# Performance work log

Measured on AMD Instinct MI355X. Metric: run time of the kernel, lower is better.

Reference implementation:

```python
import jax, jax.numpy as jnp
import numpy as np

N_NODES = 50000
N_EDGES = 1600000
NFEAT, NHID, NCLASS = 512, 128, 40


def spmm(rows, cols, vals, dense, n_rows):
    # COO sparse @ dense: gather source rows, scale, scatter-add into dest rows.
    msgs = dense[cols] * vals[:, None]            # [E, F]
    return jax.ops.segment_sum(msgs, rows, num_segments=n_rows)  # [N, F]


def setup_inputs() -> dict:
    key = jax.random.key(0)
    ks = jax.random.split(key, 10)
    s1 = 1.0 / np.sqrt(NFEAT)
    s2 = 1.0 / np.sqrt(NHID)
    return {
        "x": jax.random.normal(ks[0], (N_NODES, NFEAT), jnp.float32),
        "adj_rows": jax.random.randint(ks[1], (N_EDGES,), 0, N_NODES, jnp.int32),
        "adj_cols": jax.random.randint(ks[2], (N_EDGES,), 0, N_NODES, jnp.int32),
        "adj_vals": jax.random.uniform(ks[3], (N_EDGES,), jnp.float32) * 0.05,
        "W1": jax.random.normal(ks[4], (NFEAT, NHID), jnp.float32) * s1,
        "b1": jnp.zeros((NHID,), jnp.float32),
        "W2": jax.random.normal(ks[5], (NHID, NHID), jnp.float32) * s2,
        "b2": jnp.zeros((NHID,), jnp.float32),
        "Wout": jax.random.normal(ks[6], (NHID, NCLASS), jnp.float32) * s2,
        "bout": jnp.zeros((NCLASS,), jnp.float32),
    }


def reference(x, adj_rows, adj_cols, adj_vals, W1, b1, W2, b2, Wout, bout):
    n = x.shape[0]
    # GraphConvolution 1: support = x @ W1; out = spmm(adj, support) + b1; relu
    h = jax.nn.relu(spmm(adj_rows, adj_cols, adj_vals, x @ W1, n) + b1)
    # dropout: inference mode (training=False) -> identity
    # GraphConvolution 2 (same adjacency), relu
    h = jax.nn.relu(spmm(adj_rows, adj_cols, adj_vals, h @ W2, n) + b2)
    # output linear + log_softmax over classes
    logits = h @ Wout + bout
    return jax.nn.log_softmax(logits, axis=1)
```

## Files before the change

kernel.cpp:

```cpp
#include <hip/hip_runtime.h>

#define NFEAT 512
#define NHID 128
#define NCLASS 40
#define CAP 80

__global__ __launch_bounds__(512)
void gemm_k(const float* __restrict__ A, const float* __restrict__ B,
            float* __restrict__ C, int M, int K) {
    __shared__ float As[64][32];
    __shared__ float Bs[32][128];
    const int tid = threadIdx.x;
    const int m0  = blockIdx.x * 64;
    const int tr  = tid >> 5;
    const int tc  = tid & 31;
    const int la_r = tid >> 3;
    const int la_c = (tid & 7) << 2;
    const int lb_r = tid >> 5;
    const int lb_c = (tid & 31) << 2;

    float acc[4][4] = {};

    for (int k0 = 0; k0 < K; k0 += 32) {
        {
            int m  = m0 + la_r;
            int ms = m < M ? m : (M - 1);
            *(float4*)&As[la_r][la_c] =
                *(const float4*)(A + (size_t)ms * K + k0 + la_c);
        }
        #pragma unroll
        for (int h = 0; h < 2; ++h) {
            int kr = lb_r + h * 16;
            *(float4*)&Bs[kr][lb_c] = *(const float4*)(B + (size_t)(k0 + kr) * 128 + lb_c);
        }
        __syncthreads();

        #pragma unroll
        for (int kk = 0; kk < 8; ++kk) {
            float4 a4[4];
            #pragma unroll
            for (int i = 0; i < 4; ++i)
                a4[i] = *(const float4*)&As[tr + i * 16][kk * 4];
            #pragma unroll
            for (int kq = 0; kq < 4; ++kq) {
                const int k = kk * 4 + kq;
                float b[4];
                #pragma unroll
                for (int j = 0; j < 4; ++j) b[j] = Bs[k][tc + j * 32];
                #pragma unroll
                for (int i = 0; i < 4; ++i) {
                    const float av = (kq == 0) ? a4[i].x : (kq == 1) ? a4[i].y
                                   : (kq == 2) ? a4[i].z : a4[i].w;
                    #pragma unroll
                    for (int j = 0; j < 4; ++j)
                        acc[i][j] = fmaf(av, b[j], acc[i][j]);
                }
            }
        }
        __syncthreads();
    }

    #pragma unroll
    for (int i = 0; i < 4; ++i) {
        int m = m0 + tr + i * 16;
        if (m < M) {
            #pragma unroll
            for (int j = 0; j < 4; ++j)
                C[(size_t)m * 128 + tc + j * 32] = acc[i][j];
        }
    }
}

__global__ __launch_bounds__(256)
void build_k(const int* __restrict__ rows, const int* __restrict__ cols,
             const float* __restrict__ vals, int* __restrict__ deg,
             int2* __restrict__ ccv, int E) {
    int e = blockIdx.x * 256 + threadIdx.x;
    if (e >= E) return;
    int r = rows[e];
    int k = atomicAdd(&deg[r], 1);
    if (k < CAP)
        ccv[(size_t)r * CAP + k] = make_int2(cols[e], __float_as_int(vals[e]));
}

__global__ __launch_bounds__(256)
void hist_k(const int* __restrict__ rows, int* __restrict__ deg, int E) {
    int e = blockIdx.x * 256 + threadIdx.x;
    if (e < E) atomicAdd(&deg[rows[e]], 1);
}

__global__ __launch_bounds__(1024)
void scan_k(const int* __restrict__ deg, int* __restrict__ rowptr,
            int* __restrict__ pos, int N) {
    __shared__ int partial[1024];
    const int t = threadIdx.x;
    const int chunk = (N + 1023) >> 10;
    const int lo = t * chunk;
    const int hi = min(N, lo + chunk);
    int s = 0;
    for (int i = lo; i < hi; ++i) s += deg[i];
    partial[t] = s;
    __syncthreads();
    for (int off = 1; off < 1024; off <<= 1) {
        int v = 0;
        if (t >= off) v = partial[t - off];
        __syncthreads();
        if (t >= off) partial[t] += v;
        __syncthreads();
    }
    int base = (t == 0) ? 0 : partial[t - 1];
    for (int i = lo; i < hi; ++i) {
        rowptr[i] = base;
        pos[i]    = base;
        base += deg[i];
    }
    if (t == 0) rowptr[N] = partial[1023];
}

__global__ __launch_bounds__(256)
void scatter_k(const int* __restrict__ rows, const int* __restrict__ cols,
               const float* __restrict__ vals, int* __restrict__ pos,
               int2* __restrict__ ccv, int E) {
    int e = blockIdx.x * 256 + threadIdx.x;
    if (e >= E) return;
    int p = atomicAdd(&pos[rows[e]], 1);
    ccv[p] = make_int2(cols[e], __float_as_int(vals[e]));
}

template<bool PAD>
__global__ __launch_bounds__(256)
void spmm_mid_k(const int* __restrict__ rp, const int2* __restrict__ ccv,
                const float* __restrict__ src, const float* __restrict__ bias,
                float* __restrict__ dst, int N) {
    int row = (blockIdx.x * 256 + threadIdx.x) >> 6;
    const int lane = threadIdx.x & 63;
    if (row >= N) return;
    row = __builtin_amdgcn_readfirstlane(row);
    int start, cnt;
    if (PAD) { start = row * CAP; cnt = min(rp[row], CAP); }
    else     { start = rp[row];   cnt = rp[row + 1] - start; }
    const int2* __restrict__ p = ccv + start;
    const int fo = lane << 1;
    float2 acc = {0.f, 0.f};
    int j = 0;
    for (; j + 7 < cnt; j += 8) {
        int2 cv[8];
        #pragma unroll
        for (int u = 0; u < 8; ++u) cv[u] = p[j + u];
        float2 s[8];
        #pragma unroll
        for (int u = 0; u < 8; ++u)
            s[u] = *(const float2*)(src + (cv[u].x << 7) + fo);
        #pragma unroll
        for (int u = 0; u < 8; ++u) {
            float v = __int_as_float(cv[u].y);
            acc.x = fmaf(v, s[u].x, acc.x); acc.y = fmaf(v, s[u].y, acc.y);
        }
    }
    for (; j < cnt; ++j) {
        int2 cv = p[j];
        float v = __int_as_float(cv.y);
        float2 s = *(const float2*)(src + (cv.x << 7) + fo);
        acc.x = fmaf(v, s.x, acc.x); acc.y = fmaf(v, s.y, acc.y);
    }
    float2 bv = *(const float2*)(bias + fo);
    acc.x = fmaxf(acc.x + bv.x, 0.f);
    acc.y = fmaxf(acc.y + bv.y, 0.f);
    *(float2*)(dst + (size_t)row * NHID + fo) = acc;
}

template<bool PAD>
__global__ __launch_bounds__(256)
void spmm_out_k(const int* __restrict__ rp, const int2* __restrict__ ccv,
                const float* __restrict__ src, const float* __restrict__ b2,
                const float* __restrict__ Wout, const float* __restrict__ bout,
                float* __restrict__ out, int N) {
    __shared__ float Ws[NHID * NCLASS];
    __shared__ float hs[4][NHID];
    const int tid = threadIdx.x;
    for (int i = tid; i < NHID * NCLASS; i += 256) Ws[i] = Wout[i];
    __syncthreads();

    int row = (blockIdx.x * 256 + tid) >> 6;
    const int wave = tid >> 6, lane = tid & 63;
    if (row >= N) return;
    row = __builtin_amdgcn_readfirstlane(row);
    int start, cnt;
    if (PAD) { start = row * CAP; cnt = min(rp[row], CAP); }
    else     { start = rp[row];   cnt = rp[row + 1] - start; }
    const int2* __restrict__ p = ccv + start;
    const int fo = lane << 1;
    float2 acc = {0.f, 0.f};
    int j = 0;
    for (; j + 7 < cnt; j += 8) {
        int2 cv[8];
        #pragma unroll
        for (int u = 0; u < 8; ++u) cv[u] = p[j + u];
        float2 s[8];
        #pragma unroll
        for (int u = 0; u < 8; ++u)
            s[u] = *(const float2*)(src + (cv[u].x << 7) + fo);
        #pragma unroll
        for (int u = 0; u < 8; ++u) {
            float v = __int_as_float(cv[u].y);
            acc.x = fmaf(v, s[u].x, acc.x); acc.y = fmaf(v, s[u].y, acc.y);
        }
    }
    for (; j < cnt; ++j) {
        int2 cv = p[j];
        float v = __int_as_float(cv.y);
        float2 s = *(const float2*)(src + (cv.x << 7) + fo);
        acc.x = fmaf(v, s.x, acc.x); acc.y = fmaf(v, s.y, acc.y);
    }
    float2 bv = *(const float2*)(b2 + fo);
    hs[wave][fo]     = fmaxf(acc.x + bv.x, 0.f);
    hs[wave][fo + 1] = fmaxf(acc.y + bv.y, 0.f);

    float logit = -INFINITY;
    if (lane < NCLASS) {
        logit = bout[lane];
        #pragma unroll 4
        for (int k = 0; k < NHID; ++k)
            logit = fmaf(hs[wave][k], Ws[k * NCLASS + lane], logit);
    }
    float m = logit;
    #pragma unroll
    for (int o = 32; o > 0; o >>= 1) m = fmaxf(m, __shfl_xor(m, o));
    float e = (lane < NCLASS) ? expf(logit - m) : 0.f;
    float s = e;
    #pragma unroll
    for (int o = 32; o > 0; o >>= 1) s += __shfl_xor(s, o);
    const float lse = logf(s);
    if (lane < NCLASS)
        out[(size_t)row * NCLASS + lane] = logit - m - lse;
}

__global__ __launch_bounds__(256)
void spmm_coo_k(const int* __restrict__ rows, const int* __restrict__ cols,
                const float* __restrict__ vals, const float* __restrict__ src,
                float* __restrict__ dst, int E) {
    const long long t = (long long)blockIdx.x * 256 + threadIdx.x;
    const int e = (int)(t >> 5);
    if (e >= E) return;
    const int c = ((int)t & 31) << 2;
    const float4 s4 = *(const float4*)(src + ((size_t)cols[e] << 7) + c);
    const float v = vals[e];
    float* d = dst + ((size_t)rows[e] << 7) + c;
    unsafeAtomicAdd(d + 0, s4.x * v);
    unsafeAtomicAdd(d + 1, s4.y * v);
    unsafeAtomicAdd(d + 2, s4.z * v);
    unsafeAtomicAdd(d + 3, s4.w * v);
}

__global__ __launch_bounds__(256)
void relu_bias_k(float* __restrict__ h, const float* __restrict__ b, int total) {
    int i = blockIdx.x * 256 + threadIdx.x;
    if (i < total) h[i] = fmaxf(h[i] + b[i & (NHID - 1)], 0.f);
}

__global__ __launch_bounds__(256)
void out_k(const float* __restrict__ h2, const float* __restrict__ b2,
           const float* __restrict__ Wout, const float* __restrict__ bout,
           float* __restrict__ out, int M) {
    __shared__ float Ws[NHID * NCLASS];
    __shared__ float hs[4][NHID];
    const int tid = threadIdx.x;
    for (int i = tid; i < NHID * NCLASS; i += 256) Ws[i] = Wout[i];
    const int wave = tid >> 6, lane = tid & 63;
    const int row = blockIdx.x * 4 + wave;
    if (row < M) {
        #pragma unroll
        for (int c = lane; c < NHID; c += 64)
            hs[wave][c] = fmaxf(h2[(size_t)row * NHID + c] + b2[c], 0.f);
    }
    __syncthreads();
    if (row >= M) return;
    float acc = -INFINITY;
    if (lane < NCLASS) {
        acc = bout[lane];
        #pragma unroll 4
        for (int k = 0; k < NHID; ++k)
            acc = fmaf(hs[wave][k], Ws[k * NCLASS + lane], acc);
    }
    float m = acc;
    #pragma unroll
    for (int o = 32; o > 0; o >>= 1) m = fmaxf(m, __shfl_xor(m, o));
    float e = (lane < NCLASS) ? expf(acc - m) : 0.f;
    float s = e;
    #pragma unroll
    for (int o = 32; o > 0; o >>= 1) s += __shfl_xor(s, o);
    const float lse = logf(s);
    if (lane < NCLASS)
        out[(size_t)row * NCLASS + lane] = acc - m - lse;
}

extern "C" void kernel_launch(void* const* d_in, const int* in_sizes, int n_in,
                              void* d_out, int out_size, void* d_ws, size_t ws_size,
                              hipStream_t stream) {
    const float* x     = (const float*)d_in[0];
    const int*   arows = (const int*)  d_in[1];
    const int*   acols = (const int*)  d_in[2];
    const float* avals = (const float*)d_in[3];
    const float* W1    = (const float*)d_in[4];
    const float* b1    = (const float*)d_in[5];
    const float* W2    = (const float*)d_in[6];
    const float* b2    = (const float*)d_in[7];
    const float* Wout  = (const float*)d_in[8];
    const float* bout  = (const float*)d_in[9];
    float* out = (float*)d_out;

    const int M = in_sizes[0] / NFEAT;
    const int E = in_sizes[1];

    const size_t hbytes = (size_t)M * NHID * sizeof(float);
    char* wp = (char*)d_ws;
    float* bufA = (float*)wp;  wp += hbytes;
    float* bufB = (float*)wp;  wp += hbytes;
    int*   deg  = (int*)wp;    wp += (size_t)M * sizeof(int);
    char*  tail = wp;

    const size_t need_pad = (size_t)(tail - (char*)d_ws) + (size_t)M * CAP * sizeof(int2);
    const size_t need_csr = (size_t)(tail - (char*)d_ws) + ((size_t)M + 1 + M) * sizeof(int)
                          + (size_t)E * sizeof(int2);

    gemm_k<<<(M + 63) / 64, 512, 0, stream>>>(x, W1, bufA, M, NFEAT);

    if (need_pad <= ws_size) {
        int2* ccv = (int2*)tail;
        hipMemsetAsync(deg, 0, (size_t)M * sizeof(int), stream);
        build_k<<<(E + 255) / 256, 256, 0, stream>>>(arows, acols, avals, deg, ccv, E);
        spmm_mid_k<true><<<(M * 64 + 255) / 256, 256, 0, stream>>>(deg, ccv, bufA, b1, bufB, M);
        gemm_k<<<(M + 63) / 64, 512, 0, stream>>>(bufB, W2, bufA, M, NHID);
        spmm_out_k<true><<<(M * 64 + 255) / 256, 256, 0, stream>>>(deg, ccv, bufA, b2, Wout, bout, out, M);
    } else if (need_csr <= ws_size) {
        int* rowptr = (int*)tail;
        int* pos    = rowptr + (M + 1);
        int2* ccv   = (int2*)(pos + M);
        hipMemsetAsync(deg, 0, (size_t)M * sizeof(int), stream);
        hist_k   <<<(E + 255) / 256, 256, 0, stream>>>(arows, deg, E);
        scan_k   <<<1, 1024, 0, stream>>>(deg, rowptr, pos, M);
        scatter_k<<<(E + 255) / 256, 256, 0, stream>>>(arows, acols, avals, pos, ccv, E);
        spmm_mid_k<false><<<(M * 64 + 255) / 256, 256, 0, stream>>>(rowptr, ccv, bufA, b1, bufB, M);
        gemm_k<<<(M + 63) / 64, 512, 0, stream>>>(bufB, W2, bufA, M, NHID);
        spmm_out_k<false><<<(M * 64 + 255) / 256, 256, 0, stream>>>(rowptr, ccv, bufA, b2, Wout, bout, out, M);
    } else {
        hipMemsetAsync(bufB, 0, hbytes, stream);
        spmm_coo_k<<<(E * 32 + 255) / 256, 256, 0, stream>>>(arows, acols, avals, bufA, bufB, E);
        relu_bias_k<<<((M * NHID) + 255) / 256, 256, 0, stream>>>(bufB, b1, M * NHID);
        gemm_k<<<(M + 63) / 64, 512, 0, stream>>>(bufB, W2, bufA, M, NHID);
        hipMemsetAsync(bufB, 0, hbytes, stream);
        spmm_coo_k<<<(E * 32 + 255) / 256, 256, 0, stream>>>(arows, acols, avals, bufA, bufB, E);
        out_k<<<(M + 3) / 4, 256, 0, stream>>>(bufB, b2, Wout, bout, out, M);
    }
}
```

Baseline: 609.4 us.

## Store intermediate node features in fp16 and retile GEMM to 8x4 per thread

The intermediate feature buffers (support and hidden activations) become half precision, which halves the bytes moved by the random row gathers in both SpMM kernels and by the GEMM stores. Accumulation still happens in fp32. The GEMM drops to 256 threads, each computing an 8x4 output tile with float4 reads from shared memory, and can now load fp16 A input. The COO atomic fallback path is removed, so the CSR path becomes the unconditional fallback. This trades some accuracy for less memory traffic, and with a small workspace the fallback could now overrun it.

```diff
diff --git a/kernel.cpp b/kernel.cpp
--- a/kernel.cpp
+++ b/kernel.cpp
@@ -1,59 +1,71 @@
 #include <hip/hip_runtime.h>
+#include <hip/hip_fp16.h>
+#include <type_traits>
 
 #define NFEAT 512
 #define NHID 128
 #define NCLASS 40
 #define CAP 80
 
-__global__ __launch_bounds__(512)
-void gemm_k(const float* __restrict__ A, const float* __restrict__ B,
-            float* __restrict__ C, int M, int K) {
+template<typename TA>
+__global__ __launch_bounds__(256)
+void gemm_k(const TA* __restrict__ A, const float* __restrict__ B,
+            __half* __restrict__ C, int M, int K) {
     __shared__ float As[64][32];
     __shared__ float Bs[32][128];
     const int tid = threadIdx.x;
     const int m0  = blockIdx.x * 64;
-    const int tr  = tid >> 5;
-    const int tc  = tid & 31;
+    const int ty  = tid >> 5;
+    const int tx  = tid & 31;
     const int la_r = tid >> 3;
     const int la_c = (tid & 7) << 2;
     const int lb_r = tid >> 5;
     const int lb_c = (tid & 31) << 2;
 
-    float acc[4][4] = {};
+    float acc[8][4] = {};
 
     for (int k0 = 0; k0 < K; k0 += 32) {
-        {
-            int m  = m0 + la_r;
+        #pragma unroll
+        for (int h = 0; h < 2; ++h) {
+            int m  = m0 + la_r + h * 32;
             int ms = m < M ? m : (M - 1);
-            *(float4*)&As[la_r][la_c] =
-                *(const float4*)(A + (size_t)ms * K + k0 + la_c);
-        }
-        #pragma unroll
-        for (int h = 0; h < 2; ++h) {
-            int kr = lb_r + h * 16;
+            if constexpr (std::is_same<TA, float>::value) {
+                *(float4*)&As[la_r + h * 32][la_c] =
+                    *(const float4*)(A + (size_t)ms * K + k0 + la_c);
+            } else {
+                const __half2* ap = (const __half2*)(A + (size_t)ms * K + k0 + la_c);
+                float2 f0 = __half22float2(ap[0]);
+                float2 f1 = __half22float2(ap[1]);
+                *(float4*)&As[la_r + h * 32][la_c] = make_float4(f0.x, f0.y, f1.x, f1.y);
+            }
+        }
+        #pragma unroll
+        for (int h = 0; h < 4; ++h) {
+            int kr = lb_r + h * 8;
             *(float4*)&Bs[kr][lb_c] = *(const float4*)(B + (size_t)(k0 + kr) * 128 + lb_c);
         }
         __syncthreads();
 
         #pragma unroll
         for (int kk = 0; kk < 8; ++kk) {
-            float4 a4[4];
+            float4 a4[8];
             #pragma unroll
-            for (int i = 0; i < 4; ++i)
-                a4[i] = *(const float4*)&As[tr + i * 16][kk * 4];
+            for (int i = 0; i < 8; ++i)
+                a4[i] = *(const float4*)&As[ty * 8 + i][kk * 4];
+            float4 bb[4];
             #pragma unroll
-            for (int kq = 0; kq < 4; ++kq) {
-                const int k = kk * 4 + kq;
-                float b[4];
+            for (int q = 0; q < 4; ++q)
+                bb[q] = *(const float4*)&Bs[kk * 4 + q][tx * 4];
+            #pragma unroll
+            for (int q = 0; q < 4; ++q) {
                 #pragma unroll
-                for (int j = 0; j < 4; ++j) b[j] = Bs[k][tc + j * 32];
-                #pragma unroll
-                for (int i = 0; i < 4; ++i) {
-                    const float av = (kq == 0) ? a4[i].x : (kq == 1) ? a4[i].y
-                                   : (kq == 2) ? a4[i].z : a4[i].w;
-                    #pragma unroll
-                    for (int j = 0; j < 4; ++j)
-                        acc[i][j] = fmaf(av, b[j], acc[i][j]);
+                for (int i = 0; i < 8; ++i) {
+                    const float av = (q == 0) ? a4[i].x : (q == 1) ? a4[i].y
+                                   : (q == 2) ? a4[i].z : a4[i].w;
+                    acc[i][0] = fmaf(av, bb[q].x, acc[i][0]);
+                    acc[i][1] = fmaf(av, bb[q].y, acc[i][1]);
+                    acc[i][2] = fmaf(av, bb[q].z, acc[i][2]);
+                    acc[i][3] = fmaf(av, bb[q].w, acc[i][3]);
                 }
             }
         }
@@ -61,12 +73,15 @@
     }
 
     #pragma unroll
-    for (int i = 0; i < 4; ++i) {
-        int m = m0 + tr + i * 16;
+    for (int i = 0; i < 8; ++i) {
+        int m = m0 + ty * 8 + i;
         if (m < M) {
-            #pragma unroll
-            for (int j = 0; j < 4; ++j)
-                C[(size_t)m * 128 + tc + j * 32] = acc[i][j];
+            __half2 lo = __floats2half2_rn(acc[i][0], acc[i][1]);
+            __half2 hi = __floats2half2_rn(acc[i][2], acc[i][3]);
+            int2 pk;
+            *(__half2*)&pk.x = lo;
+            *(__half2*)&pk.y = hi;
+            *(int2*)(C + (size_t)m * 128 + tx * 4) = pk;
         }
     }
 }
@@ -130,8 +145,8 @@
 template<bool PAD>
 __global__ __launch_bounds__(256)
 void spmm_mid_k(const int* __restrict__ rp, const int2* __restrict__ ccv,
-                const float* __restrict__ src, const float* __restrict__ bias,
-                float* __restrict__ dst, int N) {
+                const __half* __restrict__ src, const float* __restrict__ bias,
+                __half* __restrict__ dst, int N) {
     int row = (blockIdx.x * 256 + threadIdx.x) >> 6;
     const int lane = threadIdx.x & 63;
     if (row >= N) return;
@@ -150,7 +165,7 @@
         float2 s[8];
         #pragma unroll
         for (int u = 0; u < 8; ++u)
-            s[u] = *(const float2*)(src + (cv[u].x << 7) + fo);
+            s[u] = __half22float2(*(const __half2*)(src + (cv[u].x << 7) + fo));
         #pragma unroll
         for (int u = 0; u < 8; ++u) {
             float v = __int_as_float(cv[u].y);
@@ -160,19 +175,19 @@
     for (; j < cnt; ++j) {
         int2 cv = p[j];
         float v = __int_as_float(cv.y);
-        float2 s = *(const float2*)(src + (cv.x << 7) + fo);
+        float2 s = __half22float2(*(const __half2*)(src + (cv.x << 7) + fo));
         acc.x = fmaf(v, s.x, acc.x); acc.y = fmaf(v, s.y, acc.y);
     }
     float2 bv = *(const float2*)(bias + fo);
     acc.x = fmaxf(acc.x + bv.x, 0.f);
     acc.y = fmaxf(acc.y + bv.y, 0.f);
-    *(float2*)(dst + (size_t)row * NHID + fo) = acc;
+    *(__half2*)(dst + (size_t)row * NHID + fo) = __floats2half2_rn(acc.x, acc.y);
 }
 
 template<bool PAD>
 __global__ __launch_bounds__(256)
 void spmm_out_k(const int* __restrict__ rp, const int2* __restrict__ ccv,
-                const float* __restrict__ src, const float* __restrict__ b2,
+                const __half* __restrict__ src, const float* __restrict__ b2,
                 const float* __restrict__ Wout, const float* __restrict__ bout,
                 float* __restrict__ out, int N) {
     __shared__ float Ws[NHID * NCLASS];
@@ -199,7 +214,7 @@
         float2 s[8];
         #pragma unroll
         for (int u = 0; u < 8; ++u)
-            s[u] = *(const float2*)(src + (cv[u].x << 7) + fo);
+            s[u] = __half22float2(*(const __half2*)(src + (cv[u].x << 7) + fo));
         #pragma unroll
         for (int u = 0; u < 8; ++u) {
             float v = __int_as_float(cv[u].y);
@@ -209,7 +224,7 @@
     for (; j < cnt; ++j) {
         int2 cv = p[j];
         float v = __int_as_float(cv.y);
-        float2 s = *(const float2*)(src + (cv.x << 7) + fo);
+        float2 s = __half22float2(*(const __half2*)(src + (cv.x << 7) + fo));
         acc.x = fmaf(v, s.x, acc.x); acc.y = fmaf(v, s.y, acc.y);
     }
     float2 bv = *(const float2*)(b2 + fo);
@@ -233,65 +248,6 @@
     const float lse = logf(s);
     if (lane < NCLASS)
         out[(size_t)row * NCLASS + lane] = logit - m - lse;
-}
-
-__global__ __launch_bounds__(256)
-void spmm_coo_k(const int* __restrict__ rows, const int* __restrict__ cols,
-                const float* __restrict__ vals, const float* __restrict__ src,
-                float* __restrict__ dst, int E) {
-    const long long t = (long long)blockIdx.x * 256 + threadIdx.x;
-    const int e = (int)(t >> 5);
-    if (e >= E) return;
-    const int c = ((int)t & 31) << 2;
-    const float4 s4 = *(const float4*)(src + ((size_t)cols[e] << 7) + c);
-    const float v = vals[e];
-    float* d = dst + ((size_t)rows[e] << 7) + c;
-    unsafeAtomicAdd(d + 0, s4.x * v);
-    unsafeAtomicAdd(d + 1, s4.y * v);
-    unsafeAtomicAdd(d + 2, s4.z * v);
-    unsafeAtomicAdd(d + 3, s4.w * v);
-}
-
-__global__ __launch_bounds__(256)
-void relu_bias_k(float* __restrict__ h, const float* __restrict__ b, int total) {
-    int i = blockIdx.x * 256 + threadIdx.x;
-    if (i < total) h[i] = fmaxf(h[i] + b[i & (NHID - 1)], 0.f);
-}
-
-__global__ __launch_bounds__(256)
-void out_k(const float* __restrict__ h2, const float* __restrict__ b2,
-           const float* __restrict__ Wout, const float* __restrict__ bout,
-           float* __restrict__ out, int M) {
-    __shared__ float Ws[NHID * NCLASS];
-    __shared__ float hs[4][NHID];
-    const int tid = threadIdx.x;
-    for (int i = tid; i < NHID * NCLASS; i += 256) Ws[i] = Wout[i];
-    const int wave = tid >> 6, lane = tid & 63;
-    const int row = blockIdx.x * 4 + wave;
-    if (row < M) {
-        #pragma unroll
-        for (int c = lane; c < NHID; c += 64)
-            hs[wave][c] = fmaxf(h2[(size_t)row * NHID + c] + b2[c], 0.f);
-    }
-    __syncthreads();
-    if (row >= M) return;
-    float acc = -INFINITY;
-    if (lane < NCLASS) {
-        acc = bout[lane];
-        #pragma unroll 4
-        for (int k = 0; k < NHID; ++k)
-            acc = fmaf(hs[wave][k], Ws[k * NCLASS + lane], acc);
-    }
-    float m = acc;
-    #pragma unroll
-    for (int o = 32; o > 0; o >>= 1) m = fmaxf(m, __shfl_xor(m, o));
-    float e = (lane < NCLASS) ? expf(acc - m) : 0.f;
-    float s = e;
-    #pragma unroll
-    for (int o = 32; o > 0; o >>= 1) s += __shfl_xor(s, o);
-    const float lse = logf(s);
-    if (lane < NCLASS)
-        out[(size_t)row * NCLASS + lane] = acc - m - lse;
 }
 
 extern "C" void kernel_launch(void* const* d_in, const int* in_sizes, int n_in,
@@ -312,27 +268,25 @@
     const int M = in_sizes[0] / NFEAT;
     const int E = in_sizes[1];
 
-    const size_t hbytes = (size_t)M * NHID * sizeof(float);
+    const size_t hbytes = (size_t)M * NHID * sizeof(__half);
     char* wp = (char*)d_ws;
-    float* bufA = (float*)wp;  wp += hbytes;
-    float* bufB = (float*)wp;  wp += hbytes;
-    int*   deg  = (int*)wp;    wp += (size_t)M * sizeof(int);
-    char*  tail = wp;
+    __half* bufA = (__half*)wp;  wp += hbytes;
+    __half* bufB = (__half*)wp;  wp += hbytes;
+    int*    deg  = (int*)wp;     wp += (size_t)M * sizeof(int);
+    char*   tail = wp;
 
     const size_t need_pad = (size_t)(tail - (char*)d_ws) + (size_t)M * CAP * sizeof(int2);
-    const size_t need_csr = (size_t)(tail - (char*)d_ws) + ((size_t)M + 1 + M) * sizeof(int)
-                          + (size_t)E * sizeof(int2);
-
-    gemm_k<<<(M + 63) / 64, 512, 0, stream>>>(x, W1, bufA, M, NFEAT);
+
+    gemm_k<float><<<(M + 63) / 64, 256, 0, stream>>>(x, W1, bufA, M, NFEAT);
 
     if (need_pad <= ws_size) {
         int2* ccv = (int2*)tail;
         hipMemsetAsync(deg, 0, (size_t)M * sizeof(int), stream);
         build_k<<<(E + 255) / 256, 256, 0, stream>>>(arows, acols, avals, deg, ccv, E);
         spmm_mid_k<true><<<(M * 64 + 255) / 256, 256, 0, stream>>>(deg, ccv, bufA, b1, bufB, M);
-        gemm_k<<<(M + 63) / 64, 512, 0, stream>>>(bufB, W2, bufA, M, NHID);
+        gemm_k<__half><<<(M + 63) / 64, 256, 0, stream>>>(bufB, W2, bufA, M, NHID);
         spmm_out_k<true><<<(M * 64 + 255) / 256, 256, 0, stream>>>(deg, ccv, bufA, b2, Wout, bout, out, M);
-    } else if (need_csr <= ws_size) {
+    } else {
         int* rowptr = (int*)tail;
         int* pos    = rowptr + (M + 1);
         int2* ccv   = (int2*)(pos + M);
@@ -341,15 +295,7 @@
         scan_k   <<<1, 1024, 0, stream>>>(deg, rowptr, pos, M);
         scatter_k<<<(E + 255) / 256, 256, 0, stream>>>(arows, acols, avals, pos, ccv, E);
         spmm_mid_k<false><<<(M * 64 + 255) / 256, 256, 0, stream>>>(rowptr, ccv, bufA, b1, bufB, M);
-        gemm_k<<<(M + 63) / 64, 512, 0, stream>>>(bufB, W2, bufA, M, NHID);
+        gemm_k<__half><<<(M + 63) / 64, 256, 0, stream>>>(bufB, W2, bufA, M, NHID);
         spmm_out_k<false><<<(M * 64 + 255) / 256, 256, 0, stream>>>(rowptr, ccv, bufA, b2, Wout, bout, out, M);
-    } else {
-        hipMemsetAsync(bufB, 0, hbytes, stream);
-        spmm_coo_k<<<(E * 32 + 255) / 256, 256, 0, stream>>>(arows, acols, avals, bufA, bufB, E);
-        relu_bias_k<<<((M * NHID) + 255) / 256, 256, 0, stream>>>(bufB, b1, M * NHID);
-        gemm_k<<<(M + 63) / 64, 512, 0, stream>>>(bufB, W2, bufA, M, NHID);
-        hipMemsetAsync(bufB, 0, hbytes, stream);
-        spmm_coo_k<<<(E * 32 + 255) / 256, 256, 0, stream>>>(arows, acols, avals, bufA, bufB, E);
-        out_k<<<(M + 3) / 4, 256, 0, stream>>>(bufB, b2, Wout, bout, out, M);
-    }
-}
+    }
+}
```

Measured after the change: 511.3 us. 16.1% less time.
